# Kernel tuning notes

Hardware: AMD Instinct MI355X
Metric: run time of the kernel (lower is better)

Reference implementation:

```python
import jax, jax.numpy as jnp
import numpy as np


def setup_inputs() -> dict:
    key = jax.random.key(0)
    k1, k2 = jax.random.split(key)
    B, L, E, K = 4, 1024, 512, 8
    xsa = jax.random.normal(k1, (B, L, E), dtype=jnp.float32)
    # attq.weight, torch Linear layout (out_features=K*E, in_features=E); scaled like a trained init
    Wq = jax.random.normal(k2, (K * E, E), dtype=jnp.float32) * 0.02
    return {"xsa": xsa, "Wq": Wq}


def reference(xsa, Wq):
    # xsa: (B, L, E); Wq: (K*E, E). attq bias, attk, and bias layers are unused in the original forward.
    B, L, E = xsa.shape
    K = Wq.shape[0] // E
    q = (xsa @ Wq.T).reshape(B, L, K, E)            # (B, L, K, E)
    # hijk = q @ xsa^T over E, per batch: (B, L, K, L)
    hijk = jnp.einsum('blke,bme->blkm', q, xsa) * (1.0 / (E ** 0.5))
    pijk = jax.nn.softmax(hijk, axis=-1)            # (B, L, K, L)
    yik = jnp.einsum('blkm,bme->blke', pijk, xsa)   # (B, L, K, E)  xsa doubles as V
    xid = yik.reshape(B, L, K * E)
    return (xid, pijk)
```

## Files before the change

### kernel.cpp

```cpp
#include <hip/hip_runtime.h>
#include <cstdint>
#include <cstddef>


typedef __bf16 bf16x8 __attribute__((ext_vector_type(8)));
typedef float f32x4 __attribute__((ext_vector_type(4)));

#define BM 128
#define BN 128
#define BK 64

__device__ __forceinline__ unsigned short f2bf(float f) {
  union { float f; unsigned int u; } x; x.f = f;
  unsigned int u = x.u;
  unsigned int r = (u + 0x7fffu + ((u >> 16) & 1u)) >> 16;
  return (unsigned short)r;
}

__device__ __forceinline__ float bf2f(unsigned short s) {
  union { unsigned int u; float f; } x; x.u = ((unsigned int)s) << 16;
  return x.f;
}

__device__ __forceinline__ void async_cp16(const void* g, void* l) {
  __builtin_amdgcn_global_load_lds(
      (const __attribute__((address_space(1))) void*)g,
      (__attribute__((address_space(3))) void*)l, 16, 0, 0);
}

template <int MODE>
__global__ __launch_bounds__(256) void gemm_nt(
    const unsigned short* __restrict__ A, const unsigned short* __restrict__ Bt,
    void* __restrict__ Cv, float* __restrict__ sums,
    int M, int N, int Kd, size_t sA, size_t sB, size_t sC, float scale) {
  __shared__ __align__(16) unsigned char smem[BM * BK * 2 + BN * BK * 2];
  unsigned short* As = (unsigned short*)smem;
  unsigned short* Bs = (unsigned short*)(smem + BM * BK * 2);

  const int tid  = threadIdx.x;
  const int lane = tid & 63;
  const int wave = tid >> 6;
  const int wm   = (wave >> 1) * 64;
  const int wn   = (wave & 1) * 64;
  const int quad = lane >> 4;
  const int lrow = lane & 15;

  const int m0 = blockIdx.x * BM;
  const int n0 = blockIdx.y * BN;
  const int b  = blockIdx.z;

  const unsigned short* Ab = A + (size_t)b * sA;
  const unsigned short* Bb = Bt + (size_t)b * sB;

  const int arow = lane >> 3;
  const int agcb = (lane & 7) ^ arow;

  f32x4 acc[4][4];
#pragma unroll
  for (int i = 0; i < 4; ++i)
#pragma unroll
    for (int j = 0; j < 4; ++j) acc[i][j] = (f32x4){0.f, 0.f, 0.f, 0.f};

  for (int k0 = 0; k0 < Kd; k0 += BK) {
    __syncthreads();
#pragma unroll
    for (int t = 0; t < 4; ++t) {
      int c = wave * 4 + t;
      async_cp16(Ab + (size_t)(m0 + c * 8 + arow) * Kd + k0 + agcb * 8,
                 As + c * 512);
    }
#pragma unroll
    for (int t = 0; t < 4; ++t) {
      int c = wave * 4 + t;
      async_cp16(Bb + (size_t)(n0 + c * 8 + arow) * Kd + k0 + agcb * 8,
                 Bs + c * 512);
    }
    __syncthreads();
#pragma unroll
    for (int ks = 0; ks < BK; ks += 32) {
      bf16x8 af[4], bfr[4];
#pragma unroll
      for (int i = 0; i < 4; ++i) {
        int r = wm + i * 16 + lrow;
        int cb = (ks >> 3) + quad;
        af[i] = *(const bf16x8*)&As[r * 64 + ((cb ^ (r & 7)) << 3)];
      }
#pragma unroll
      for (int j = 0; j < 4; ++j) {
        int r = wn + j * 16 + lrow;
        int cb = (ks >> 3) + quad;
        bfr[j] = *(const bf16x8*)&Bs[r * 64 + ((cb ^ (r & 7)) << 3)];
      }
#pragma unroll
      for (int i = 0; i < 4; ++i)
#pragma unroll
        for (int j = 0; j < 4; ++j)
          acc[i][j] = __builtin_amdgcn_mfma_f32_16x16x32_bf16(af[i], bfr[j], acc[i][j], 0, 0, 0);
    }
  }

  float linv[4][4];
  if constexpr (MODE == 2) {
#pragma unroll
    for (int i = 0; i < 4; ++i)
#pragma unroll
      for (int r = 0; r < 4; ++r)
        linv[i][r] = 1.0f / sums[(size_t)b * M + m0 + wm + i * 16 + quad * 4 + r];
  }
  __syncthreads();
  float* epi = (float*)smem;
  const int erow = (wm ? 16 : 0) + quad * 4;
#pragma unroll
  for (int i = 0; i < 4; ++i) {
#pragma unroll
    for (int j = 0; j < 4; ++j)
#pragma unroll
      for (int r = 0; r < 4; ++r) {
        float v = acc[i][j][r];
        if constexpr (MODE == 0) v *= scale;
        if constexpr (MODE == 1) v = __expf(v * scale);
        if constexpr (MODE == 2) v *= linv[i][r];
        epi[(erow + r) * 132 + wn + j * 16 + lrow] = v;
      }
    __syncthreads();
    if constexpr (MODE <= 1) {
      unsigned short* C = (unsigned short*)Cv + (size_t)b * sC;
      int trow = tid >> 4, tcol = (tid & 15) * 8;
#pragma unroll
      for (int rep = 0; rep < 2; ++rep) {
        int lr = trow + rep * 16;
        int grow = m0 + i * 16 + lr + (lr >= 16 ? 48 : 0);
        float vals[8];
#pragma unroll
        for (int u = 0; u < 8; ++u) vals[u] = epi[lr * 132 + tcol + u];
        union { unsigned short s[8]; uint4 v; } pk;
#pragma unroll
        for (int u = 0; u < 8; ++u) pk.s[u] = f2bf(vals[u]);
        *(uint4*)&C[(size_t)grow * N + n0 + tcol] = pk.v;
        if constexpr (MODE == 1) {
          float s = 0.f;
#pragma unroll
          for (int u = 0; u < 8; ++u) s += vals[u];
          s += __shfl_xor(s, 1);
          s += __shfl_xor(s, 2);
          s += __shfl_xor(s, 4);
          s += __shfl_xor(s, 8);
          if ((tid & 15) == 0)
            atomicAdd(&sums[(size_t)b * M + grow], s);
        }
      }
    } else {
      float* C = (float*)Cv + (size_t)b * sC;
      int trow = tid >> 5, tcol = (tid & 31) * 4;
#pragma unroll
      for (int rep = 0; rep < 4; ++rep) {
        int lr = trow + rep * 8;
        int grow = m0 + i * 16 + lr + (lr >= 16 ? 48 : 0);
        *(float4*)&C[(size_t)grow * N + n0 + tcol] = *(const float4*)&epi[lr * 132 + tcol];
      }
    }
    __syncthreads();
  }
}

__global__ __launch_bounds__(256) void cvt_f32_to_bf16(
    const float* __restrict__ in, unsigned short* __restrict__ out, int n4) {
  int i = blockIdx.x * blockDim.x + threadIdx.x;
  if (i < n4) {
    float4 v = *(const float4*)(in + (size_t)i * 4);
    union { unsigned short s[4]; uint2 v2; } pk;
    pk.s[0] = f2bf(v.x); pk.s[1] = f2bf(v.y);
    pk.s[2] = f2bf(v.z); pk.s[3] = f2bf(v.w);
    *(uint2*)(out + (size_t)i * 4) = pk.v2;
  }
}

__global__ __launch_bounds__(256) void transpose_to_bf16(
    const float* __restrict__ in, unsigned short* __restrict__ out, int L, int E) {
  __shared__ unsigned short tile[32][33];
  int b  = blockIdx.z;
  int e0 = blockIdx.x * 32;
  int l0 = blockIdx.y * 32;
  int tx = threadIdx.x & 31;
  int ty = threadIdx.x >> 5;
  const float* inb = in + (size_t)b * L * E;
#pragma unroll
  for (int r = 0; r < 32; r += 8)
    tile[ty + r][tx] = f2bf(inb[(size_t)(l0 + ty + r) * E + e0 + tx]);
  __syncthreads();
  unsigned short* outb = out + (size_t)b * L * E;
#pragma unroll
  for (int r = 0; r < 32; r += 8)
    outb[(size_t)(e0 + ty + r) * L + l0 + tx] = tile[tx][ty + r];
}

__global__ __launch_bounds__(256) void normalize_rows(
    const unsigned short* __restrict__ Pu, const float* __restrict__ sums,
    float* __restrict__ P) {
  size_t row = blockIdx.x;
  int t = threadIdx.x;
  float inv = 1.0f / sums[row];
  uint2 u = *(const uint2*)(Pu + row * 1024 + t * 4);
  float4 o;
  o.x = bf2f((unsigned short)(u.x & 0xffff)) * inv;
  o.y = bf2f((unsigned short)(u.x >> 16)) * inv;
  o.z = bf2f((unsigned short)(u.y & 0xffff)) * inv;
  o.w = bf2f((unsigned short)(u.y >> 16)) * inv;
  *(float4*)(P + row * 1024 + t * 4) = o;
}

extern "C" void kernel_launch(void* const* d_in, const int* in_sizes, int n_in,
                              void* d_out, int out_size, void* d_ws, size_t ws_size,
                              hipStream_t stream) {
  const float* xsa = (const float*)d_in[0];
  const float* Wq  = (const float*)d_in[1];
  float* out = (float*)d_out;

  const int Bn = 4, L = 1024, E = 512, K = 8;
  const int M1 = Bn * L;
  const int N1 = K * E;
  const int M2 = L * K;
  const size_t xid_n = (size_t)Bn * L * K * E;

  float* xid  = out;
  float* pijk = out + xid_n;

  unsigned short* ws   = (unsigned short*)d_ws;
  unsigned short* WqB  = ws;
  unsigned short* xsaB = WqB + (size_t)N1 * E;
  unsigned short* xsaT = xsaB + (size_t)Bn * L * E;
  unsigned short* QB   = xsaT + (size_t)Bn * L * E;
  unsigned short* PuB  = QB + (size_t)M1 * N1;
  float* sums = (float*)(PuB + (size_t)Bn * M2 * L);

  {
    int n4 = (N1 * E) / 4;
    cvt_f32_to_bf16<<<dim3((n4 + 255) / 256), dim3(256), 0, stream>>>(Wq, WqB, n4);
    int m4 = (Bn * L * E) / 4;
    cvt_f32_to_bf16<<<dim3((m4 + 255) / 256), dim3(256), 0, stream>>>(xsa, xsaB, m4);
    transpose_to_bf16<<<dim3(E / 32, L / 32, Bn), dim3(256), 0, stream>>>(xsa, xsaT, L, E);
    hipMemsetAsync(sums, 0, (size_t)Bn * M2 * sizeof(float), stream);
  }

  gemm_nt<0><<<dim3(M1 / BM, N1 / BN, 1), dim3(256), 0, stream>>>(
      xsaB, WqB, QB, nullptr, M1, N1, E, 0, 0, 0, 1.0f);

  gemm_nt<1><<<dim3(M2 / BM, L / BN, Bn), dim3(256), 0, stream>>>(
      QB, xsaB, PuB, sums, M2, L, E,
      (size_t)M2 * E, (size_t)L * E, (size_t)M2 * L, 0.04419417382415922f);

  normalize_rows<<<dim3(Bn * M2), dim3(256), 0, stream>>>(PuB, sums, pijk);

  gemm_nt<2><<<dim3(M2 / BM, E / BN, Bn), dim3(256), 0, stream>>>(
      PuB, xsaT, xid, sums, M2, E, L,
      (size_t)M2 * L, (size_t)E * L, (size_t)M2 * E, 1.0f);
}
```

Before: 351.3 us.

## Use 256x256 double-buffered GEMM tiles with interleaved MFMA and fused conversion kernels

Replaces the 128x128 single-buffered GEMM with a 256x256-tile, 512-thread kernel. It double-buffers LDS so async global-to-LDS loads of the next K slice overlap MFMA work on the current one, interleaving LDS fragment reads and compute under raw barriers and s_setprio. It also merges the xsa bf16 conversion and transpose into one kernel and widens normalize_rows to 8 elements per thread. Larger tiles cut global traffic per FLOP, but they raise register and LDS pressure (128KB LDS with launch_bounds(512,2)) and leave fewer blocks for the small GEMMs.

```diff
diff --git a/kernel.cpp b/kernel.cpp
--- a/kernel.cpp
+++ b/kernel.cpp
@@ -5,10 +5,6 @@
 
 typedef __bf16 bf16x8 __attribute__((ext_vector_type(8)));
 typedef float f32x4 __attribute__((ext_vector_type(4)));
-
-#define BM 128
-#define BN 128
-#define BK 64
 
 __device__ __forceinline__ unsigned short f2bf(float f) {
   union { float f; unsigned int u; } x; x.f = f;
@@ -28,138 +24,185 @@
       (__attribute__((address_space(3))) void*)l, 16, 0, 0);
 }
 
+__device__ __forceinline__ void barrier_raw() {
+  asm volatile("" ::: "memory");
+  __builtin_amdgcn_s_barrier();
+  asm volatile("" ::: "memory");
+}
+
 template <int MODE>
-__global__ __launch_bounds__(256) void gemm_nt(
+__global__ __launch_bounds__(512, 2) void gemm_nt256(
     const unsigned short* __restrict__ A, const unsigned short* __restrict__ Bt,
     void* __restrict__ Cv, float* __restrict__ sums,
     int M, int N, int Kd, size_t sA, size_t sB, size_t sC, float scale) {
-  __shared__ __align__(16) unsigned char smem[BM * BK * 2 + BN * BK * 2];
-  unsigned short* As = (unsigned short*)smem;
-  unsigned short* Bs = (unsigned short*)(smem + BM * BK * 2);
+  __shared__ __align__(16) unsigned short smem[2 * 2 * 256 * 64];
 
   const int tid  = threadIdx.x;
   const int lane = tid & 63;
   const int wave = tid >> 6;
-  const int wm   = (wave >> 1) * 64;
-  const int wn   = (wave & 1) * 64;
+  const int wm   = (wave >> 2) * 128;
+  const int wn   = (wave & 3) * 64;
   const int quad = lane >> 4;
   const int lrow = lane & 15;
 
-  const int m0 = blockIdx.x * BM;
-  const int n0 = blockIdx.y * BN;
+  const int m0 = blockIdx.x * 256;
+  const int n0 = blockIdx.y * 256;
   const int b  = blockIdx.z;
 
   const unsigned short* Ab = A + (size_t)b * sA;
   const unsigned short* Bb = Bt + (size_t)b * sB;
 
   const int arow = lane >> 3;
-  const int agcb = (lane & 7) ^ arow;
-
-  f32x4 acc[4][4];
-#pragma unroll
-  for (int i = 0; i < 4; ++i)
+  const int acb  = (lane & 7) ^ arow;
+  const unsigned short* pA[4];
+  const unsigned short* pB[4];
+#pragma unroll
+  for (int i = 0; i < 4; ++i) {
+    const int c = i * 8 + wave;
+    pA[i] = Ab + (size_t)(m0 + c * 8 + arow) * Kd + acb * 8;
+    pB[i] = Bb + (size_t)(n0 + c * 8 + arow) * Kd + acb * 8;
+  }
+
+  auto stageA = [&](unsigned short* dst, int k0) {
+#pragma unroll
+    for (int i = 0; i < 4; ++i)
+      async_cp16(pA[i] + k0, dst + (i * 8 + wave) * 512);
+  };
+  auto stageB = [&](unsigned short* dst, int k0) {
+#pragma unroll
+    for (int i = 0; i < 4; ++i)
+      async_cp16(pB[i] + k0, dst + (i * 8 + wave) * 512);
+  };
+
+  const int xo0 = ((0 + quad) ^ (lrow & 7)) << 3;
+  const int xo1 = ((4 + quad) ^ (lrow & 7)) << 3;
+
+  f32x4 acc[8][4];
+#pragma unroll
+  for (int i = 0; i < 8; ++i)
 #pragma unroll
     for (int j = 0; j < 4; ++j) acc[i][j] = (f32x4){0.f, 0.f, 0.f, 0.f};
 
-  for (int k0 = 0; k0 < Kd; k0 += BK) {
-    __syncthreads();
-#pragma unroll
-    for (int t = 0; t < 4; ++t) {
-      int c = wave * 4 + t;
-      async_cp16(Ab + (size_t)(m0 + c * 8 + arow) * Kd + k0 + agcb * 8,
-                 As + c * 512);
+  bf16x8 a[4][2];
+  bf16x8 bb[4][2];
+
+  auto rdA = [&](int mq, const unsigned short* As_) {
+#pragma unroll
+    for (int f = 0; f < 4; ++f) {
+      const int r = wm + mq * 64 + f * 16 + lrow;
+      a[f][0] = *(const bf16x8*)&As_[r * 64 + xo0];
+      a[f][1] = *(const bf16x8*)&As_[r * 64 + xo1];
     }
-#pragma unroll
-    for (int t = 0; t < 4; ++t) {
-      int c = wave * 4 + t;
-      async_cp16(Bb + (size_t)(n0 + c * 8 + arow) * Kd + k0 + agcb * 8,
-                 Bs + c * 512);
+  };
+  auto rdB = [&](int nq, const unsigned short* Bs_) {
+#pragma unroll
+    for (int f = 0; f < 2; ++f) {
+      const int r = wn + nq * 32 + f * 16 + lrow;
+      bb[nq * 2 + f][0] = *(const bf16x8*)&Bs_[r * 64 + xo0];
+      bb[nq * 2 + f][1] = *(const bf16x8*)&Bs_[r * 64 + xo1];
+    }
+  };
+  auto mm = [&](int mq, int nq) {
+    __builtin_amdgcn_s_setprio(1);
+#pragma unroll
+    for (int ks = 0; ks < 2; ++ks)
+#pragma unroll
+      for (int f = 0; f < 4; ++f)
+#pragma unroll
+        for (int g = 0; g < 2; ++g)
+          acc[mq * 4 + f][nq * 2 + g] = __builtin_amdgcn_mfma_f32_16x16x32_bf16(
+              a[f][ks], bb[nq * 2 + g][ks], acc[mq * 4 + f][nq * 2 + g], 0, 0, 0);
+    __builtin_amdgcn_s_setprio(0);
+  };
+
+  stageA(smem, 0);
+  stageB(smem + 16384, 0);
+  asm volatile("s_waitcnt vmcnt(0)" ::: "memory");
+  barrier_raw();
+
+  const int nt = Kd >> 6;
+  for (int t = 0; t < nt; ++t) {
+    const int cur = t & 1;
+    const unsigned short* As_ = smem + cur * 32768;
+    const unsigned short* Bs_ = As_ + 16384;
+    unsigned short* An  = smem + ((cur ^ 1) * 32768);
+    unsigned short* Bn_ = An + 16384;
+    const bool pf = (t + 1 < nt);
+    const int k1 = (t + 1) << 6;
+
+    rdA(0, As_);
+    rdB(0, Bs_);
+    if (pf) stageA(An, k1);
+    barrier_raw();
+    mm(0, 0);
+    barrier_raw();
+
+    rdB(1, Bs_);
+    if (pf) stageB(Bn_, k1);
+    barrier_raw();
+    mm(0, 1);
+    barrier_raw();
+
+    rdA(1, As_);
+    barrier_raw();
+    mm(1, 1);
+    barrier_raw();
+
+    mm(1, 0);
+    asm volatile("s_waitcnt vmcnt(0)" ::: "memory");
+    barrier_raw();
+  }
+
+  float* epi = (float*)smem;
+  const int wmo = wm ? 16 : 0;
+  const int erb = wmo + quad * 4;
+#pragma unroll
+  for (int fm = 0; fm < 8; ++fm) {
+    float linv[4];
+    if constexpr (MODE == 2) {
+#pragma unroll
+      for (int r = 0; r < 4; ++r)
+        linv[r] = 1.0f / sums[(size_t)b * M + m0 + wm + fm * 16 + quad * 4 + r];
     }
     __syncthreads();
 #pragma unroll
-    for (int ks = 0; ks < BK; ks += 32) {
-      bf16x8 af[4], bfr[4];
-#pragma unroll
-      for (int i = 0; i < 4; ++i) {
-        int r = wm + i * 16 + lrow;
-        int cb = (ks >> 3) + quad;
-        af[i] = *(const bf16x8*)&As[r * 64 + ((cb ^ (r & 7)) << 3)];
-      }
-#pragma unroll
-      for (int j = 0; j < 4; ++j) {
-        int r = wn + j * 16 + lrow;
-        int cb = (ks >> 3) + quad;
-        bfr[j] = *(const bf16x8*)&Bs[r * 64 + ((cb ^ (r & 7)) << 3)];
-      }
-#pragma unroll
-      for (int i = 0; i < 4; ++i)
-#pragma unroll
-        for (int j = 0; j < 4; ++j)
-          acc[i][j] = __builtin_amdgcn_mfma_f32_16x16x32_bf16(af[i], bfr[j], acc[i][j], 0, 0, 0);
-    }
-  }
-
-  float linv[4][4];
-  if constexpr (MODE == 2) {
-#pragma unroll
-    for (int i = 0; i < 4; ++i)
-#pragma unroll
-      for (int r = 0; r < 4; ++r)
-        linv[i][r] = 1.0f / sums[(size_t)b * M + m0 + wm + i * 16 + quad * 4 + r];
-  }
-  __syncthreads();
-  float* epi = (float*)smem;
-  const int erow = (wm ? 16 : 0) + quad * 4;
-#pragma unroll
-  for (int i = 0; i < 4; ++i) {
-#pragma unroll
-    for (int j = 0; j < 4; ++j)
+    for (int fn = 0; fn < 4; ++fn)
 #pragma unroll
       for (int r = 0; r < 4; ++r) {
-        float v = acc[i][j][r];
+        float v = acc[fm][fn][r];
         if constexpr (MODE == 0) v *= scale;
         if constexpr (MODE == 1) v = __expf(v * scale);
-        if constexpr (MODE == 2) v *= linv[i][r];
-        epi[(erow + r) * 132 + wn + j * 16 + lrow] = v;
+        if constexpr (MODE == 2) v *= linv[r];
+        epi[(erb + r) * 260 + wn + fn * 16 + lrow] = v;
       }
     __syncthreads();
-    if constexpr (MODE <= 1) {
-      unsigned short* C = (unsigned short*)Cv + (size_t)b * sC;
-      int trow = tid >> 4, tcol = (tid & 15) * 8;
-#pragma unroll
-      for (int rep = 0; rep < 2; ++rep) {
-        int lr = trow + rep * 16;
-        int grow = m0 + i * 16 + lr + (lr >= 16 ? 48 : 0);
-        float vals[8];
-#pragma unroll
-        for (int u = 0; u < 8; ++u) vals[u] = epi[lr * 132 + tcol + u];
-        union { unsigned short s[8]; uint4 v; } pk;
-#pragma unroll
-        for (int u = 0; u < 8; ++u) pk.s[u] = f2bf(vals[u]);
-        *(uint4*)&C[(size_t)grow * N + n0 + tcol] = pk.v;
+#pragma unroll
+    for (int rep = 0; rep < 4; ++rep) {
+      const int lr = (tid >> 6) + rep * 8;
+      const int gr = m0 + fm * 16 + (lr & 15) + (lr >= 16 ? 128 : 0);
+      const int c4 = (tid & 63) * 4;
+      float4 v4 = *(const float4*)&epi[lr * 260 + c4];
+      if constexpr (MODE <= 1) {
+        unsigned short* C = (unsigned short*)Cv + (size_t)b * sC;
+        union { unsigned short s[4]; uint2 u; } pk;
+        pk.s[0] = f2bf(v4.x); pk.s[1] = f2bf(v4.y);
+        pk.s[2] = f2bf(v4.z); pk.s[3] = f2bf(v4.w);
+        *(uint2*)&C[(size_t)gr * N + n0 + c4] = pk.u;
         if constexpr (MODE == 1) {
-          float s = 0.f;
-#pragma unroll
-          for (int u = 0; u < 8; ++u) s += vals[u];
+          float s = v4.x + v4.y + v4.z + v4.w;
           s += __shfl_xor(s, 1);
           s += __shfl_xor(s, 2);
           s += __shfl_xor(s, 4);
           s += __shfl_xor(s, 8);
-          if ((tid & 15) == 0)
-            atomicAdd(&sums[(size_t)b * M + grow], s);
+          s += __shfl_xor(s, 16);
+          s += __shfl_xor(s, 32);
+          if (lane == 0) atomicAdd(&sums[(size_t)b * M + gr], s);
         }
-      }
-    } else {
-      float* C = (float*)Cv + (size_t)b * sC;
-      int trow = tid >> 5, tcol = (tid & 31) * 4;
-#pragma unroll
-      for (int rep = 0; rep < 4; ++rep) {
-        int lr = trow + rep * 8;
-        int grow = m0 + i * 16 + lr + (lr >= 16 ? 48 : 0);
-        *(float4*)&C[(size_t)grow * N + n0 + tcol] = *(const float4*)&epi[lr * 132 + tcol];
+      } else {
+        float* C = (float*)Cv + (size_t)b * sC;
+        *(float4*)&C[(size_t)gr * N + n0 + c4] = v4;
       }
     }
-    __syncthreads();
   }
 }
 
@@ -175,8 +218,9 @@
   }
 }
 
-__global__ __launch_bounds__(256) void transpose_to_bf16(
-    const float* __restrict__ in, unsigned short* __restrict__ out, int L, int E) {
+__global__ __launch_bounds__(256) void cvt_and_transpose_bf16(
+    const float* __restrict__ in, unsigned short* __restrict__ outS,
+    unsigned short* __restrict__ outT, int L, int E) {
   __shared__ unsigned short tile[32][33];
   int b  = blockIdx.z;
   int e0 = blockIdx.x * 32;
@@ -184,29 +228,39 @@
   int tx = threadIdx.x & 31;
   int ty = threadIdx.x >> 5;
   const float* inb = in + (size_t)b * L * E;
+  unsigned short* outSb = outS + (size_t)b * L * E;
+#pragma unroll
+  for (int r = 0; r < 32; r += 8) {
+    unsigned short v = f2bf(inb[(size_t)(l0 + ty + r) * E + e0 + tx]);
+    tile[ty + r][tx] = v;
+    outSb[(size_t)(l0 + ty + r) * E + e0 + tx] = v;
+  }
+  __syncthreads();
+  unsigned short* outTb = outT + (size_t)b * L * E;
 #pragma unroll
   for (int r = 0; r < 32; r += 8)
-    tile[ty + r][tx] = f2bf(inb[(size_t)(l0 + ty + r) * E + e0 + tx]);
-  __syncthreads();
-  unsigned short* outb = out + (size_t)b * L * E;
-#pragma unroll
-  for (int r = 0; r < 32; r += 8)
-    outb[(size_t)(e0 + ty + r) * L + l0 + tx] = tile[tx][ty + r];
+    outTb[(size_t)(e0 + ty + r) * L + l0 + tx] = tile[tx][ty + r];
 }
 
 __global__ __launch_bounds__(256) void normalize_rows(
     const unsigned short* __restrict__ Pu, const float* __restrict__ sums,
-    float* __restrict__ P) {
-  size_t row = blockIdx.x;
-  int t = threadIdx.x;
-  float inv = 1.0f / sums[row];
-  uint2 u = *(const uint2*)(Pu + row * 1024 + t * 4);
-  float4 o;
-  o.x = bf2f((unsigned short)(u.x & 0xffff)) * inv;
-  o.y = bf2f((unsigned short)(u.x >> 16)) * inv;
-  o.z = bf2f((unsigned short)(u.y & 0xffff)) * inv;
-  o.w = bf2f((unsigned short)(u.y >> 16)) * inv;
-  *(float4*)(P + row * 1024 + t * 4) = o;
+    float* __restrict__ P, int total8) {
+  int i = blockIdx.x * 256 + threadIdx.x;
+  if (i >= total8) return;
+  size_t base = (size_t)i * 8;
+  float inv = 1.0f / sums[base >> 10];
+  uint4 u = *(const uint4*)(Pu + base);
+  float4 o0, o1;
+  o0.x = bf2f((unsigned short)(u.x & 0xffff)) * inv;
+  o0.y = bf2f((unsigned short)(u.x >> 16)) * inv;
+  o0.z = bf2f((unsigned short)(u.y & 0xffff)) * inv;
+  o0.w = bf2f((unsigned short)(u.y >> 16)) * inv;
+  o1.x = bf2f((unsigned short)(u.z & 0xffff)) * inv;
+  o1.y = bf2f((unsigned short)(u.z >> 16)) * inv;
+  o1.z = bf2f((unsigned short)(u.w & 0xffff)) * inv;
+  o1.w = bf2f((unsigned short)(u.w >> 16)) * inv;
+  *(float4*)(P + base) = o0;
+  *(float4*)(P + base + 4) = o1;
 }
 
 extern "C" void kernel_launch(void* const* d_in, const int* in_sizes, int n_in,
@@ -236,22 +290,24 @@
   {
     int n4 = (N1 * E) / 4;
     cvt_f32_to_bf16<<<dim3((n4 + 255) / 256), dim3(256), 0, stream>>>(Wq, WqB, n4);
-    int m4 = (Bn * L * E) / 4;
-    cvt_f32_to_bf16<<<dim3((m4 + 255) / 256), dim3(256), 0, stream>>>(xsa, xsaB, m4);
-    transpose_to_bf16<<<dim3(E / 32, L / 32, Bn), dim3(256), 0, stream>>>(xsa, xsaT, L, E);
+    cvt_and_transpose_bf16<<<dim3(E / 32, L / 32, Bn), dim3(256), 0, stream>>>(
+        xsa, xsaB, xsaT, L, E);
     hipMemsetAsync(sums, 0, (size_t)Bn * M2 * sizeof(float), stream);
   }
 
-  gemm_nt<0><<<dim3(M1 / BM, N1 / BN, 1), dim3(256), 0, stream>>>(
+  gemm_nt256<0><<<dim3(M1 / 256, N1 / 256, 1), dim3(512), 0, stream>>>(
       xsaB, WqB, QB, nullptr, M1, N1, E, 0, 0, 0, 1.0f);
 
-  gemm_nt<1><<<dim3(M2 / BM, L / BN, Bn), dim3(256), 0, stream>>>(
+  gemm_nt256<1><<<dim3(M2 / 256, L / 256, Bn), dim3(512), 0, stream>>>(
       QB, xsaB, PuB, sums, M2, L, E,
       (size_t)M2 * E, (size_t)L * E, (size_t)M2 * L, 0.04419417382415922f);
 
-  normalize_rows<<<dim3(Bn * M2), dim3(256), 0, stream>>>(PuB, sums, pijk);
-
-  gemm_nt<2><<<dim3(M2 / BM, E / BN, Bn), dim3(256), 0, stream>>>(
+  {
+    int total8 = (int)((size_t)Bn * M2 * L / 8);
+    normalize_rows<<<dim3(total8 / 256), dim3(256), 0, stream>>>(PuB, sums, pijk, total8);
+  }
+
+  gemm_nt256<2><<<dim3(M2 / 256, E / 256, Bn), dim3(512), 0, stream>>>(
       PuB, xsaT, xid, sums, M2, E, L,
       (size_t)M2 * L, (size_t)E * L, (size_t)M2 * E, 1.0f);
 }
```

Measured after the change: 325.6 us. 1.08x faster.
